# Performance work log

Hardware: AMD Instinct MI355X
Metric: run time of the kernel (lower is better)

The kernel has to match this reference:

```python
import jax, jax.numpy as jnp
import numpy as np

B, L, D = 2, 2048, 1024
N_HEADS, N_KV_HEADS = 16, 4
HEAD_DIM = D // N_HEADS
WINDOW = 1024
ROPE_BASE = 10000.0


def setup_inputs() -> dict:
    key = jax.random.key(0)
    ks = jax.random.split(key, 5)
    s = 0.02
    return {
        "x": jax.random.normal(ks[0], (B, L, D), jnp.float32),
        "Wq": jax.random.normal(ks[1], (D, N_HEADS * HEAD_DIM), jnp.float32) * s,
        "Wk": jax.random.normal(ks[2], (D, N_KV_HEADS * HEAD_DIM), jnp.float32) * s,
        "Wv": jax.random.normal(ks[3], (D, N_KV_HEADS * HEAD_DIM), jnp.float32) * s,
        "Wo": jax.random.normal(ks[4], (N_HEADS * HEAD_DIM, D), jnp.float32) * s,
    }


def _rope_cos_sin(seq_len, head_dim, dtype):
    inv_freq = 1.0 / (ROPE_BASE ** (jnp.arange(0, head_dim, 2, dtype=jnp.float32) / head_dim))
    angles = jnp.arange(seq_len, dtype=jnp.float32)[:, None] * inv_freq[None, :]  # [L, d/2]
    emb = jnp.concatenate([angles, angles], axis=-1)  # [L, d]
    return jnp.cos(emb).astype(dtype), jnp.sin(emb).astype(dtype)


def _rotate_half(t):
    t1, t2 = jnp.split(t, 2, axis=-1)
    return jnp.concatenate([-t2, t1], axis=-1)


def reference(x, Wq, Wk, Wv, Wo):
    b, l, d = x.shape
    q = (x @ Wq).reshape(b, l, N_HEADS, HEAD_DIM).transpose(0, 2, 1, 3)      # [B,H,L,d]
    k = (x @ Wk).reshape(b, l, N_KV_HEADS, HEAD_DIM).transpose(0, 2, 1, 3)   # [B,Kv,L,d]
    v = (x @ Wv).reshape(b, l, N_KV_HEADS, HEAD_DIM).transpose(0, 2, 1, 3)

    cos, sin = _rope_cos_sin(l, HEAD_DIM, x.dtype)  # [L,d]
    q = q * cos[None, None] + _rotate_half(q) * sin[None, None]
    k = k * cos[None, None] + _rotate_half(k) * sin[None, None]

    # GQA: expand kv heads to query heads
    group = N_HEADS // N_KV_HEADS
    k = jnp.repeat(k, group, axis=1)  # [B,H,L,d]
    v = jnp.repeat(v, group, axis=1)

    scale = 1.0 / np.sqrt(HEAD_DIM)
    scores = jnp.einsum("bhqd,bhkd->bhqk", q, k) * scale  # [B,H,L,L]

    # sliding-window causal mask: attend to j with j <= i and i - j < WINDOW
    i = jnp.arange(l)[:, None]
    j = jnp.arange(l)[None, :]
    allowed = (j <= i) & (i - j < WINDOW)
    scores = jnp.where(allowed[None, None], scores, jnp.finfo(scores.dtype).min)

    attn = jax.nn.softmax(scores, axis=-1)
    out = jnp.einsum("bhqk,bhkd->bhqd", attn, v)           # [B,H,L,d]
    out = out.transpose(0, 2, 1, 3).reshape(b, l, N_HEADS * HEAD_DIM)
    return out @ Wo  # [B,L,D]; dropout p=0 is identity
```

## Files before the change

### kernel.cpp

```cpp
#include <hip/hip_runtime.h>

typedef unsigned short u16;
typedef unsigned int u32;
typedef short short8 __attribute__((ext_vector_type(8)));
typedef float f32x4 __attribute__((ext_vector_type(4)));

#define N_B 2
#define N_L 2048
#define N_D 1024
#define N_H 16
#define N_KVH 4
#define HDIM 64
#define WINDOW 1024

#define QSCALE (0.125f * 1.44269504088896f)

__device__ __forceinline__ u16 f2bf(float f) {
  unsigned u = __builtin_bit_cast(unsigned, f);
  u = u + 0x7fffu + ((u >> 16) & 1u);
  return (u16)(u >> 16);
}

__device__ __forceinline__ u32 pk2bf(float lo, float hi) {
  u32 a = __builtin_bit_cast(u32, lo) + 0x8000u;
  u32 b = __builtin_bit_cast(u32, hi) + 0x8000u;
  return __builtin_amdgcn_perm(b, a, 0x07060302u);
}

__device__ __forceinline__ void gl2lds16(const u16* g, u16* l) {
  __builtin_amdgcn_global_load_lds((const __attribute__((address_space(1))) void*)g,
                                   (__attribute__((address_space(3))) void*)l, 16, 0, 0);
}


__global__ __launch_bounds__(256) void prep_kernel(
    const float* __restrict__ x, const float* __restrict__ Wq, const float* __restrict__ Wk,
    const float* __restrict__ Wv, const float* __restrict__ Wo,
    u16* __restrict__ xb, u16* __restrict__ wqkvT, u16* __restrict__ woT,
    float* __restrict__ rc, float* __restrict__ rs) {
  __shared__ float tbuf[32][33];
  int bid = blockIdx.x, tid = threadIdx.x;
  if (bid < 1024) {
    size_t base = ((size_t)bid * 256 + tid) * 16;
    u32 o[8];
#pragma unroll
    for (int j = 0; j < 4; j++) {
      float4 f = *(const float4*)&x[base + j * 4];
      o[2 * j] = pk2bf(f.x, f.y);
      o[2 * j + 1] = pk2bf(f.z, f.w);
    }
    *(uint4*)&xb[base] = *(uint4*)&o[0];
    *(uint4*)&xb[base + 8] = *(uint4*)&o[4];
  } else if (bid < 3584) {
    const float* src;
    u16* dst;
    int gx, t, shift;
    if (bid < 2048) { src = Wq; dst = wqkvT; gx = 32; shift = 5; t = bid - 1024; }
    else if (bid < 2304) { src = Wk; dst = wqkvT + 1024 * 1024; gx = 8; shift = 3; t = bid - 2048; }
    else if (bid < 2560) { src = Wv; dst = wqkvT + 1280 * 1024; gx = 8; shift = 3; t = bid - 2304; }
    else { src = Wo; dst = woT; gx = 32; shift = 5; t = bid - 2560; }
    int srcN = gx * 32;
    int n0 = (t & (gx - 1)) * 32, k0 = (t >> shift) * 32;
    int lx = tid & 31, ly = tid >> 5;
#pragma unroll
    for (int q = 0; q < 4; q++)
      tbuf[ly + 8 * q][lx] = src[(k0 + ly + 8 * q) * srcN + n0 + lx];
    __syncthreads();
#pragma unroll
    for (int q = 0; q < 4; q++)
      dst[(n0 + ly + 8 * q) * 1024 + k0 + lx] = f2bf(tbuf[lx][ly + 8 * q]);
  } else {
    int idx = (bid - 3584) * 256 + tid;
    int i = idx >> 5, j = idx & 31;
    float inv = powf(10000.0f, -(float)j * (1.0f / 32.0f));
    float ang = (float)i * inv;
    rc[idx] = cosf(ang);
    rs[idx] = sinf(ang);
  }
}


template <int MODE>
__global__ __launch_bounds__(256, 2) void gemm_kernel(
    const u16* __restrict__ A, const u16* __restrict__ Bt,
    u16* __restrict__ qo, u16* __restrict__ ko, u16* __restrict__ vo,
    float* __restrict__ fo, const float* __restrict__ rc, const float* __restrict__ rs) {
  __shared__ u16 smem[65536 / 2];
  int tid = threadIdx.x;
  int w = tid >> 6, lane = tid & 63, quad = lane >> 4, r = lane & 15;
  int rx = r & 7;
  int wm = w >> 1, wn = w & 1;
  int m0 = blockIdx.y * 128, n0 = blockIdx.x * 128;

  f32x4 acc[4][4];
#pragma unroll
  for (int a_ = 0; a_ < 4; a_++)
#pragma unroll
    for (int b_ = 0; b_ < 4; b_++) acc[a_][b_] = {0.f, 0.f, 0.f, 0.f};

  auto stage = [&](int kt, int buf) {
    u16* a_s = smem + buf * 8192;
    u16* b_s = smem + 16384 + buf * 8192;
#pragma unroll
    for (int it = 0; it < 4; ++it) {
      int cc = it * 256 + tid;
      int row = cc >> 3, p = cc & 7, c = p ^ (row & 7);
      gl2lds16(&A[(size_t)(m0 + row) * 1024 + kt * 64 + c * 8], &a_s[cc * 8]);
    }
#pragma unroll
    for (int it = 0; it < 4; ++it) {
      int cc = it * 256 + tid;
      int row = cc >> 3, p = cc & 7, c = p ^ (row & 7);
      gl2lds16(&Bt[(size_t)(n0 + row) * 1024 + kt * 64 + c * 8], &b_s[cc * 8]);
    }
  };

  stage(0, 0);
  for (int kt = 0; kt < 16; ++kt) {
    int buf = kt & 1;
    __syncthreads();
    if (kt + 1 < 16) stage(kt + 1, buf ^ 1);
    u16* a_s = smem + buf * 8192;
    u16* b_s = smem + 16384 + buf * 8192;
#pragma unroll
    for (int ks = 0; ks < 2; ks++) {
      int pc = (ks * 4 + quad) ^ rx;
      short8 af[4], bfr[4];
#pragma unroll
      for (int tm = 0; tm < 4; tm++)
        af[tm] = *(const short8*)&a_s[(wm * 64 + tm * 16 + r) * 64 + pc * 8];
#pragma unroll
      for (int tn = 0; tn < 4; tn++)
        bfr[tn] = *(const short8*)&b_s[(wn * 64 + tn * 16 + r) * 64 + pc * 8];
#pragma unroll
      for (int tm = 0; tm < 4; tm++)
#pragma unroll
        for (int tn = 0; tn < 4; tn++)
          acc[tm][tn] = __builtin_amdgcn_mfma_f32_16x16x32_bf16(af[tm], bfr[tn], acc[tm][tn], 0, 0, 0);
    }
  }

  int nbase = n0 + wn * 64;
  if constexpr (MODE == 0) {
    if (nbase < 1024) {
      int h = nbase >> 6;
#pragma unroll
      for (int tm = 0; tm < 4; tm++) {
#pragma unroll
        for (int reg = 0; reg < 4; reg++) {
          int m = m0 + wm * 64 + tm * 16 + quad * 4 + reg;
          int b = m >> 11, i = m & 2047;
          size_t base = ((size_t)(b * N_H + h) * N_L + i) * HDIM;
#pragma unroll
          for (int tn = 0; tn < 2; tn++) {
            int dlo = tn * 16 + r;
            float c = rc[i * 32 + dlo], s = rs[i * 32 + dlo];
            float vlo = acc[tm][tn][reg], vhi = acc[tm][tn + 2][reg];
            qo[base + dlo] = f2bf((vlo * c - vhi * s) * QSCALE);
            qo[base + dlo + 32] = f2bf((vhi * c + vlo * s) * QSCALE);
          }
        }
      }
    } else if (nbase < 1280) {
      int h = (nbase - 1024) >> 6;
#pragma unroll
      for (int tm = 0; tm < 4; tm++) {
#pragma unroll
        for (int reg = 0; reg < 4; reg++) {
          int m = m0 + wm * 64 + tm * 16 + quad * 4 + reg;
          int b = m >> 11, i = m & 2047;
          size_t base = ((size_t)(b * N_KVH + h) * N_L + i) * HDIM;
#pragma unroll
          for (int tn = 0; tn < 2; tn++) {
            int dlo = tn * 16 + r;
            float c = rc[i * 32 + dlo], s = rs[i * 32 + dlo];
            float vlo = acc[tm][tn][reg], vhi = acc[tm][tn + 2][reg];
            ko[base + dlo] = f2bf(vlo * c - vhi * s);
            ko[base + dlo + 32] = f2bf(vhi * c + vlo * s);
          }
        }
      }
    } else {
      __syncthreads();
      int hkv = (nbase - 1280) >> 6;
      int bb = (m0 + wm * 64) >> 11;
      int tbase = (m0 + wm * 64) & 2047;
      u16* myvs = smem + w * 4608;
#pragma unroll
      for (int tm = 0; tm < 4; tm++) {
#pragma unroll
        for (int tn = 0; tn < 4; tn++) {
          uint2 pk;
          pk.x = pk2bf(acc[tm][tn][0], acc[tm][tn][1]);
          pk.y = pk2bf(acc[tm][tn][2], acc[tm][tn][3]);
          *(uint2*)&myvs[(tn * 16 + r) * 72 + tm * 16 + quad * 4] = pk;
        }
      }
      __asm__ volatile("s_waitcnt lgkmcnt(0)" ::: "memory");
      u16* vtb = vo + (size_t)((bb * N_KVH + hkv) * 64) * 2048;
#pragma unroll
      for (int q2 = 0; q2 < 8; ++q2) {
        int flat = q2 * 64 + lane;
        int row = flat >> 3, part = flat & 7;
        uint4 val = *(uint4*)&myvs[row * 72 + part * 8];
        *(uint4*)&vtb[row * 2048 + tbase + part * 8] = val;
      }
    }
  } else {
#pragma unroll
    for (int tm = 0; tm < 4; tm++) {
#pragma unroll
      for (int reg = 0; reg < 4; reg++) {
        int m = m0 + wm * 64 + tm * 16 + quad * 4 + reg;
#pragma unroll
        for (int tn = 0; tn < 4; tn++)
          fo[(size_t)m * 1024 + nbase + tn * 16 + r] = acc[tm][tn][reg];
      }
    }
  }
}


__global__ __launch_bounds__(256) void attn_kernel(
    const u16* __restrict__ Q, const u16* __restrict__ K,
    const u16* __restrict__ Vt, u16* __restrict__ O) {
  __shared__ u16 k_s[2][64 * 64];
  __shared__ u16 v_s[2][64 * 64];
  __shared__ u16 pt[4][16 * 64];
  int tid = threadIdx.x, w = tid >> 6, lane = tid & 63, quad = lane >> 4, r = lane & 15;
  int qb = 31 - blockIdx.x;
  int h = blockIdx.y, b = blockIdx.z;
  int i0 = qb * 64;
  int hk = h >> 2;
  int qw0 = i0 + w * 16;
  int iq = qw0 + r;

  const u16* qptr = Q + (size_t)((b * N_H + h) * N_L + iq) * HDIM;
  short8 qf[2];
  qf[0] = *(const short8*)&qptr[quad * 8];
  qf[1] = *(const short8*)&qptr[32 + quad * 8];

  const u16* kbase = K + (size_t)(b * N_KVH + hk) * N_L * HDIM;
  const u16* vtbase = Vt + (size_t)(b * N_KVH + hk) * HDIM * N_L;

  auto stage = [&](int jt, int buf) {
#pragma unroll
    for (int it = 0; it < 2; ++it) {
      int cc = it * 256 + tid;
      int row = cc >> 3, p = cc & 7, c = p ^ (row & 7);
      gl2lds16(&kbase[(size_t)(jt * 64 + row) * 64 + c * 8], &k_s[buf][cc * 8]);
    }
#pragma unroll
    for (int it = 0; it < 2; ++it) {
      int cc = it * 256 + tid;
      int row = cc >> 3, p = cc & 7, c = p ^ (row & 7);
      gl2lds16(&vtbase[(size_t)row * 2048 + jt * 64 + c * 8], &v_s[buf][cc * 8]);
    }
  };

  float l_lane = 0.f;
  f32x4 o_acc[4];
#pragma unroll
  for (int tm = 0; tm < 4; tm++) o_acc[tm] = {0.f, 0.f, 0.f, 0.f};

  int jt0 = (i0 >= WINDOW) ? ((i0 - (WINDOW - 1)) >> 6) : 0;
  int nt = qb - jt0 + 1;
  u16* mypt = pt[w];
  int rx = r & 7;

  stage(jt0, 0);

  for (int t = 0; t < nt; ++t) {
    int jt = jt0 + t, j0 = jt << 6, buf = t & 1;
    __syncthreads();
    if (t + 1 < nt) stage(jt + 1, buf ^ 1);

    f32x4 s_acc[4];
#pragma unroll
    for (int tm = 0; tm < 4; tm++) s_acc[tm] = {0.f, 0.f, 0.f, 0.f};
#pragma unroll
    for (int ks = 0; ks < 2; ks++) {
      int pc = (ks * 4 + quad) ^ rx;
#pragma unroll
      for (int tm = 0; tm < 4; tm++) {
        short8 kf = *(const short8*)&k_s[buf][(tm * 16 + r) * 64 + pc * 8];
        s_acc[tm] = __builtin_amdgcn_mfma_f32_16x16x32_bf16(kf, qf[ks], s_acc[tm], 0, 0, 0);
      }
    }

    bool interior = (j0 + 63 <= qw0) && (qw0 + 15 - j0 < WINDOW);
    if (!interior) {
#pragma unroll
      for (int tm = 0; tm < 4; tm++) {
#pragma unroll
        for (int reg = 0; reg < 4; reg++) {
          int j = j0 + tm * 16 + quad * 4 + reg;
          bool ok = (j <= iq) && (iq - j < WINDOW);
          if (!ok) s_acc[tm][reg] = -1e30f;
        }
      }
    }

    float p[4][4];
#pragma unroll
    for (int tm = 0; tm < 4; tm++)
#pragma unroll
      for (int reg = 0; reg < 4; reg++) {
        float e = __builtin_amdgcn_exp2f(s_acc[tm][reg]);
        p[tm][reg] = e;
        l_lane += e;
      }

#pragma unroll
    for (int tm = 0; tm < 4; tm++) {
      uint2 pk;
      pk.x = pk2bf(p[tm][0], p[tm][1]);
      pk.y = pk2bf(p[tm][2], p[tm][3]);
      int c = tm * 2 + (quad >> 1), half = quad & 1;
      int pp = c ^ rx;
      *(uint2*)&mypt[r * 64 + pp * 8 + half * 4] = pk;
    }
    __asm__ volatile("s_waitcnt lgkmcnt(0)" ::: "memory");

#pragma unroll
    for (int ks = 0; ks < 2; ks++) {
      int pc = (ks * 4 + quad) ^ rx;
      short8 bp = *(const short8*)&mypt[r * 64 + pc * 8];
#pragma unroll
      for (int tm = 0; tm < 4; tm++) {
        short8 av = *(const short8*)&v_s[buf][(tm * 16 + r) * 64 + pc * 8];
        o_acc[tm] = __builtin_amdgcn_mfma_f32_16x16x32_bf16(av, bp, o_acc[tm], 0, 0, 0);
      }
    }
  }

  l_lane += __shfl_xor(l_lane, 16);
  l_lane += __shfl_xor(l_lane, 32);
  float inv = 1.0f / l_lane;
  size_t obase = (size_t)(b * N_L + iq) * 1024 + h * 64;
#pragma unroll
  for (int tm = 0; tm < 4; tm++) {
    uint2 pk;
    pk.x = pk2bf(o_acc[tm][0] * inv, o_acc[tm][1] * inv);
    pk.y = pk2bf(o_acc[tm][2] * inv, o_acc[tm][3] * inv);
    *(uint2*)&O[obase + tm * 16 + quad * 4] = pk;
  }
}


extern "C" void kernel_launch(void* const* d_in, const int* in_sizes, int n_in,
                              void* d_out, int out_size, void* d_ws, size_t ws_size,
                              hipStream_t stream) {
  const float* x = (const float*)d_in[0];
  const float* Wq = (const float*)d_in[1];
  const float* Wk = (const float*)d_in[2];
  const float* Wv = (const float*)d_in[3];
  const float* Wo = (const float*)d_in[4];
  float* out = (float*)d_out;
  char* ws = (char*)d_ws;

  u16* xb    = (u16*)(ws);
  u16* wqkvT = (u16*)(ws + 0x800000);
  u16* woT   = (u16*)(ws + 0xB00000);
  u16* Qb    = (u16*)(ws + 0xD00000);
  u16* Kb    = (u16*)(ws + 0x1500000);
  u16* Vtb   = (u16*)(ws + 0x1700000);
  u16* Ob    = (u16*)(ws + 0x1900000);
  float* rc  = (float*)(ws + 0x2100000);
  float* rs  = (float*)(ws + 0x2140000);

  prep_kernel<<<3840, 256, 0, stream>>>(x, Wq, Wk, Wv, Wo, xb, wqkvT, woT, rc, rs);
  gemm_kernel<0><<<dim3(12, 32), 256, 0, stream>>>(xb, wqkvT, Qb, Kb, Vtb, nullptr, rc, rs);
  attn_kernel<<<dim3(32, 16, 2), 256, 0, stream>>>(Qb, Kb, Vtb, Ob);
  gemm_kernel<1><<<dim3(8, 32), 256, 0, stream>>>(Ob, woT, nullptr, nullptr, nullptr, out, nullptr, nullptr);
}
```

Before: 147.8 us.

## Double query rows per attention block to reuse each staged K/V tile

Each attention workgroup now covers 128 query rows instead of 64, with every wave handling two 16-row query fragments that share the same K and V LDS reads and tiles. This halves the number of blocks and the global-to-LDS staging traffic per query row, and per-wave tiles outside the causal/window range are skipped. In exchange there are fewer blocks (512), more registers per thread, a larger P scratch buffer, and some wasted staging at block edges where waves sit idle.

```diff
diff --git a/kernel.cpp b/kernel.cpp
--- a/kernel.cpp
+++ b/kernel.cpp
@@ -226,19 +226,22 @@
     const u16* __restrict__ Vt, u16* __restrict__ O) {
   __shared__ u16 k_s[2][64 * 64];
   __shared__ u16 v_s[2][64 * 64];
-  __shared__ u16 pt[4][16 * 64];
+  __shared__ u16 pt[4][32 * 64];
   int tid = threadIdx.x, w = tid >> 6, lane = tid & 63, quad = lane >> 4, r = lane & 15;
-  int qb = 31 - blockIdx.x;
+  int qb = 15 - blockIdx.x;
   int h = blockIdx.y, b = blockIdx.z;
-  int i0 = qb * 64;
+  int i0 = qb * 128;
   int hk = h >> 2;
-  int qw0 = i0 + w * 16;
-  int iq = qw0 + r;
-
-  const u16* qptr = Q + (size_t)((b * N_H + h) * N_L + iq) * HDIM;
-  short8 qf[2];
-  qf[0] = *(const short8*)&qptr[quad * 8];
-  qf[1] = *(const short8*)&qptr[32 + quad * 8];
+  int qw0 = i0 + w * 32;
+  int rx = r & 7;
+
+  short8 qf[2][2];
+#pragma unroll
+  for (int qi = 0; qi < 2; qi++) {
+    const u16* qptr = Q + (size_t)((b * N_H + h) * N_L + qw0 + qi * 16 + r) * HDIM;
+    qf[qi][0] = *(const short8*)&qptr[quad * 8];
+    qf[qi][1] = *(const short8*)&qptr[32 + quad * 8];
+  }
 
   const u16* kbase = K + (size_t)(b * N_KVH + hk) * N_L * HDIM;
   const u16* vtbase = Vt + (size_t)(b * N_KVH + hk) * HDIM * N_L;
@@ -258,15 +261,17 @@
     }
   };
 
-  float l_lane = 0.f;
-  f32x4 o_acc[4];
-#pragma unroll
-  for (int tm = 0; tm < 4; tm++) o_acc[tm] = {0.f, 0.f, 0.f, 0.f};
+  float l0 = 0.f, l1 = 0.f;
+  f32x4 o_acc[4][2];
+#pragma unroll
+  for (int tm = 0; tm < 4; tm++) {
+    o_acc[tm][0] = {0.f, 0.f, 0.f, 0.f};
+    o_acc[tm][1] = {0.f, 0.f, 0.f, 0.f};
+  }
 
   int jt0 = (i0 >= WINDOW) ? ((i0 - (WINDOW - 1)) >> 6) : 0;
-  int nt = qb - jt0 + 1;
+  int nt = 2 * qb + 2 - jt0;
   u16* mypt = pt[w];
-  int rx = r & 7;
 
   stage(jt0, 0);
 
@@ -275,75 +280,101 @@
     __syncthreads();
     if (t + 1 < nt) stage(jt + 1, buf ^ 1);
 
-    f32x4 s_acc[4];
-#pragma unroll
-    for (int tm = 0; tm < 4; tm++) s_acc[tm] = {0.f, 0.f, 0.f, 0.f};
+    if (j0 > qw0 + 31 || j0 + 63 < qw0 - (WINDOW - 1)) continue;
+
+    f32x4 s_acc[4][2];
+#pragma unroll
+    for (int tm = 0; tm < 4; tm++) {
+      s_acc[tm][0] = {0.f, 0.f, 0.f, 0.f};
+      s_acc[tm][1] = {0.f, 0.f, 0.f, 0.f};
+    }
 #pragma unroll
     for (int ks = 0; ks < 2; ks++) {
       int pc = (ks * 4 + quad) ^ rx;
 #pragma unroll
       for (int tm = 0; tm < 4; tm++) {
         short8 kf = *(const short8*)&k_s[buf][(tm * 16 + r) * 64 + pc * 8];
-        s_acc[tm] = __builtin_amdgcn_mfma_f32_16x16x32_bf16(kf, qf[ks], s_acc[tm], 0, 0, 0);
-      }
-    }
-
-    bool interior = (j0 + 63 <= qw0) && (qw0 + 15 - j0 < WINDOW);
+        s_acc[tm][0] = __builtin_amdgcn_mfma_f32_16x16x32_bf16(kf, qf[0][ks], s_acc[tm][0], 0, 0, 0);
+        s_acc[tm][1] = __builtin_amdgcn_mfma_f32_16x16x32_bf16(kf, qf[1][ks], s_acc[tm][1], 0, 0, 0);
+      }
+    }
+
+    bool interior = (j0 + 63 <= qw0) && (qw0 + 31 - j0 < WINDOW);
     if (!interior) {
 #pragma unroll
       for (int tm = 0; tm < 4; tm++) {
 #pragma unroll
-        for (int reg = 0; reg < 4; reg++) {
-          int j = j0 + tm * 16 + quad * 4 + reg;
-          bool ok = (j <= iq) && (iq - j < WINDOW);
-          if (!ok) s_acc[tm][reg] = -1e30f;
+        for (int qi = 0; qi < 2; qi++) {
+          int iqx = qw0 + qi * 16 + r;
+#pragma unroll
+          for (int reg = 0; reg < 4; reg++) {
+            int j = j0 + tm * 16 + quad * 4 + reg;
+            bool ok = (j <= iqx) && (iqx - j < WINDOW);
+            if (!ok) s_acc[tm][qi][reg] = -1e30f;
+          }
         }
       }
     }
 
-    float p[4][4];
 #pragma unroll
     for (int tm = 0; tm < 4; tm++)
 #pragma unroll
       for (int reg = 0; reg < 4; reg++) {
-        float e = __builtin_amdgcn_exp2f(s_acc[tm][reg]);
-        p[tm][reg] = e;
-        l_lane += e;
+        float e0 = __builtin_amdgcn_exp2f(s_acc[tm][0][reg]);
+        s_acc[tm][0][reg] = e0;
+        l0 += e0;
+        float e1 = __builtin_amdgcn_exp2f(s_acc[tm][1][reg]);
+        s_acc[tm][1][reg] = e1;
+        l1 += e1;
       }
 
 #pragma unroll
     for (int tm = 0; tm < 4; tm++) {
-      uint2 pk;
-      pk.x = pk2bf(p[tm][0], p[tm][1]);
-      pk.y = pk2bf(p[tm][2], p[tm][3]);
-      int c = tm * 2 + (quad >> 1), half = quad & 1;
-      int pp = c ^ rx;
-      *(uint2*)&mypt[r * 64 + pp * 8 + half * 4] = pk;
+      int pp = (tm * 2 + (quad >> 1)) ^ rx;
+      int half4 = (quad & 1) * 4;
+      uint2 pk0;
+      pk0.x = pk2bf(s_acc[tm][0][0], s_acc[tm][0][1]);
+      pk0.y = pk2bf(s_acc[tm][0][2], s_acc[tm][0][3]);
+      *(uint2*)&mypt[r * 64 + pp * 8 + half4] = pk0;
+      uint2 pk1;
+      pk1.x = pk2bf(s_acc[tm][1][0], s_acc[tm][1][1]);
+      pk1.y = pk2bf(s_acc[tm][1][2], s_acc[tm][1][3]);
+      *(uint2*)&mypt[(16 + r) * 64 + pp * 8 + half4] = pk1;
     }
     __asm__ volatile("s_waitcnt lgkmcnt(0)" ::: "memory");
 
 #pragma unroll
     for (int ks = 0; ks < 2; ks++) {
       int pc = (ks * 4 + quad) ^ rx;
-      short8 bp = *(const short8*)&mypt[r * 64 + pc * 8];
+      short8 bp0 = *(const short8*)&mypt[r * 64 + pc * 8];
+      short8 bp1 = *(const short8*)&mypt[(16 + r) * 64 + pc * 8];
 #pragma unroll
       for (int tm = 0; tm < 4; tm++) {
         short8 av = *(const short8*)&v_s[buf][(tm * 16 + r) * 64 + pc * 8];
-        o_acc[tm] = __builtin_amdgcn_mfma_f32_16x16x32_bf16(av, bp, o_acc[tm], 0, 0, 0);
-      }
-    }
-  }
-
-  l_lane += __shfl_xor(l_lane, 16);
-  l_lane += __shfl_xor(l_lane, 32);
-  float inv = 1.0f / l_lane;
-  size_t obase = (size_t)(b * N_L + iq) * 1024 + h * 64;
+        o_acc[tm][0] = __builtin_amdgcn_mfma_f32_16x16x32_bf16(av, bp0, o_acc[tm][0], 0, 0, 0);
+        o_acc[tm][1] = __builtin_amdgcn_mfma_f32_16x16x32_bf16(av, bp1, o_acc[tm][1], 0, 0, 0);
+      }
+    }
+  }
+
+  l0 += __shfl_xor(l0, 16);
+  l0 += __shfl_xor(l0, 32);
+  l1 += __shfl_xor(l1, 16);
+  l1 += __shfl_xor(l1, 32);
+  float inv0 = 1.0f / l0;
+  float inv1 = 1.0f / l1;
+  size_t ob0 = (size_t)(b * N_L + qw0 + r) * 1024 + h * 64;
+  size_t ob1 = (size_t)(b * N_L + qw0 + 16 + r) * 1024 + h * 64;
 #pragma unroll
   for (int tm = 0; tm < 4; tm++) {
-    uint2 pk;
-    pk.x = pk2bf(o_acc[tm][0] * inv, o_acc[tm][1] * inv);
-    pk.y = pk2bf(o_acc[tm][2] * inv, o_acc[tm][3] * inv);
-    *(uint2*)&O[obase + tm * 16 + quad * 4] = pk;
+    uint2 pk0;
+    pk0.x = pk2bf(o_acc[tm][0][0] * inv0, o_acc[tm][0][1] * inv0);
+    pk0.y = pk2bf(o_acc[tm][0][2] * inv0, o_acc[tm][0][3] * inv0);
+    *(uint2*)&O[ob0 + tm * 16 + quad * 4] = pk0;
+    uint2 pk1;
+    pk1.x = pk2bf(o_acc[tm][1][0] * inv1, o_acc[tm][1][1] * inv1);
+    pk1.y = pk2bf(o_acc[tm][1][2] * inv1, o_acc[tm][1][3] * inv1);
+    *(uint2*)&O[ob1 + tm * 16 + quad * 4] = pk1;
   }
 }
 
@@ -371,6 +402,6 @@
 
   prep_kernel<<<3840, 256, 0, stream>>>(x, Wq, Wk, Wv, Wo, xb, wqkvT, woT, rc, rs);
   gemm_kernel<0><<<dim3(12, 32), 256, 0, stream>>>(xb, wqkvT, Qb, Kb, Vtb, nullptr, rc, rs);
-  attn_kernel<<<dim3(32, 16, 2), 256, 0, stream>>>(Qb, Kb, Vtb, Ob);
+  attn_kernel<<<dim3(16, 16, 2), 256, 0, stream>>>(Qb, Kb, Vtb, Ob);
   gemm_kernel<1><<<dim3(8, 32), 256, 0, stream>>>(Ob, woT, nullptr, nullptr, nullptr, out, nullptr, nullptr);
 }
```

Result: slower. 152.3 us (+3.0%).
